# Optimization experiments

Hardware: AMD Instinct MI355X
Metric: run time of the kernel (lower is better)

The kernel has to match this reference:

```python
import jax, jax.numpy as jnp
import numpy as np


def setup_inputs() -> dict:
    key = jax.random.key(0)
    k1, k2, k3, k4, k5 = jax.random.split(key, 5)
    B, N, E, C, O = 4, 10000, 32, 128, 128
    x = jax.random.normal(k1, (B, N, C), dtype=jnp.float32)
    idx = jax.random.randint(k2, (B, N, E), 0, N)
    drop = jax.random.uniform(k3, (B, N, E)) < 0.1
    edge_index = jnp.where(drop, -1, idx).astype(jnp.int64)
    W = jax.random.normal(k4, (2 * C, O), dtype=jnp.float32) * (1.0 / np.sqrt(2 * C))
    b = jax.random.normal(k5, (O,), dtype=jnp.float32) * 0.01
    return {"x": x, "edge_index": edge_index, "W": W, "b": b}


def reference(x, edge_index, W, b):
    B, N, C = x.shape
    E = edge_index.shape[-1]
    # pad a zero node row; -1 indices point at it (torch negative-index semantics)
    padded = jnp.concatenate([x, jnp.zeros((B, 1, C), dtype=x.dtype)], axis=1)  # [B, N+1, C]
    idx = jnp.where(edge_index < 0, N, edge_index)
    neigh = jax.vmap(lambda p, i: p[i])(padded, idx)  # [B, N, E, C]
    x_e = jnp.broadcast_to(x[:, :, None, :], (B, N, E, C))
    feat = jnp.concatenate([x_e, neigh - x_e], axis=-1)  # [B, N, E, 2C]
    h = jax.nn.elu(jnp.einsum('bnec,co->bneo', feat, W) + b)  # [B, N, E, O]
    h = jnp.where((edge_index != -1)[..., None], h, -jnp.inf)
    return jnp.max(h, axis=2)  # [B, N, O]
```

## Files before the change

kernel.cpp:

```cpp
#include <hip/hip_runtime.h>
#include <math.h>

#define BATCH 4
#define NNODE 10000
#define EDIM  32
#define CDIM  128
#define ODIM  128
#define MTOT  (BATCH * NNODE)

typedef __attribute__((ext_vector_type(8))) short bf16x8;
typedef __attribute__((ext_vector_type(4))) float f32x4;

__device__ __forceinline__ unsigned short f2bf(float f) {
    unsigned u = __float_as_uint(f);
    u += 0x7fffu + ((u >> 16) & 1u);
    return (unsigned short)(u >> 16);
}

__global__ __launch_bounds__(256) void prep_w(
    const float* __restrict__ W, unsigned short* __restrict__ Bcat)
{
    int gid = blockIdx.x * 256 + threadIdx.x;
    int n = gid >> 7;
    int k = gid & 127;
    float v;
    if (n < 128) v = W[(size_t)k * ODIM + n] - W[(size_t)(k + 128) * ODIM + n];
    else         v = W[(size_t)(k + 128) * ODIM + (n - 128)];
    Bcat[(size_t)n * CDIM + k] = f2bf(v);
}

__global__ __launch_bounds__(256) void gemm_mfma(
    const float* __restrict__ x,
    const unsigned short* __restrict__ Bcat,
    const float* __restrict__ bias,
    float* __restrict__ U,
    unsigned short* __restrict__ T)
{
    const int m0   = blockIdx.x * 64;
    const int wv   = threadIdx.x >> 6;
    const int lane = threadIdx.x & 63;
    const int l16  = lane & 15;
    const int quad = lane >> 4;
    const int nq   = wv * 64;

    f32x4 acc[4][4];
    #pragma unroll
    for (int i = 0; i < 4; i++)
        #pragma unroll
        for (int j = 0; j < 4; j++) acc[i][j] = (f32x4){0.f, 0.f, 0.f, 0.f};

    const float* xb = x + (size_t)m0 * CDIM;

    #pragma unroll
    for (int ks = 0; ks < 4; ks++) {
        const int kb = ks * 32 + quad * 8;

        bf16x8 bfr[4];
        #pragma unroll
        for (int ct = 0; ct < 4; ct++)
            bfr[ct] = *(const bf16x8*)(Bcat + (size_t)(nq + ct * 16 + l16) * CDIM + kb);

        bf16x8 afr[4];
        #pragma unroll
        for (int rt = 0; rt < 4; rt++) {
            const float* ap = xb + (size_t)(rt * 16 + l16) * CDIM + kb;
            float4 a0 = *(const float4*)ap;
            float4 a1 = *(const float4*)(ap + 4);
            bf16x8 v;
            v[0] = (short)f2bf(a0.x); v[1] = (short)f2bf(a0.y);
            v[2] = (short)f2bf(a0.z); v[3] = (short)f2bf(a0.w);
            v[4] = (short)f2bf(a1.x); v[5] = (short)f2bf(a1.y);
            v[6] = (short)f2bf(a1.z); v[7] = (short)f2bf(a1.w);
            afr[rt] = v;
        }

        #pragma unroll
        for (int rt = 0; rt < 4; rt++)
            #pragma unroll
            for (int ct = 0; ct < 4; ct++)
                acc[rt][ct] = __builtin_amdgcn_mfma_f32_16x16x32_bf16(
                    afr[rt], bfr[ct], acc[rt][ct], 0, 0, 0);
    }

    if (wv < 2) {
        #pragma unroll
        for (int ct = 0; ct < 4; ct++) {
            int n = nq + ct * 16 + l16;
            float bb = bias[n];
            #pragma unroll
            for (int rt = 0; rt < 4; rt++) {
                int row = m0 + rt * 16 + quad * 4;
                #pragma unroll
                for (int r = 0; r < 4; r++)
                    U[(size_t)(row + r) * ODIM + n] = acc[rt][ct][r] + bb;
            }
        }
    } else {
        #pragma unroll
        for (int ct = 0; ct < 4; ct++) {
            int n = nq - 128 + ct * 16 + l16;
            #pragma unroll
            for (int rt = 0; rt < 4; rt++) {
                int row = m0 + rt * 16 + quad * 4;
                #pragma unroll
                for (int r = 0; r < 4; r++)
                    T[(size_t)(row + r) * ODIM + n] = f2bf(acc[rt][ct][r]);
            }
        }
    }
}

__global__ __launch_bounds__(256) void gather_max(
    const int* __restrict__ idx,
    const float* Uin,
    const unsigned short* __restrict__ T,
    float* out)
{
    const int g    = blockIdx.x;
    const int b    = (g & 7) >> 1;
    const int wb   = (g >> 3) * 2 + (g & 1);
    const int wave = threadIdx.x >> 6;
    const int lane = threadIdx.x & 63;
    const int node = b * NNODE + wb * 4 + wave;

    __shared__ int sidx[4][EDIM];
    if (threadIdx.x < 4 * EDIM) {
        int w = threadIdx.x >> 5;
        int e = threadIdx.x & 31;
        sidx[w][e] = idx[(size_t)(b * NNODE + wb * 4 + w) * EDIM + e];
    }
    __syncthreads();

    const unsigned short* tb = T + (size_t)b * NNODE * ODIM;
    const int o2 = lane * 2;

    int      jv[EDIM];
    unsigned vv[EDIM];
    #pragma unroll
    for (int e = 0; e < EDIM; e++) {
        int j = sidx[wave][e];
        jv[e] = j;
        int jc = j < 0 ? 0 : j;
        vv[e] = *(const unsigned*)(tb + (size_t)jc * ODIM + o2);
    }

    float m0 = -INFINITY, m1 = -INFINITY;
    bool any = false;
    #pragma unroll
    for (int e = 0; e < EDIM; e++) {
        if (jv[e] >= 0) {
            any = true;
            m0 = fmaxf(m0, __uint_as_float(vv[e] << 16));
            m1 = fmaxf(m1, __uint_as_float(vv[e] & 0xffff0000u));
        }
    }

    float2 uv = *(const float2*)&Uin[(size_t)node * ODIM + o2];
    float r0, r1;
    if (any) {
        float s0 = uv.x + m0;
        float s1 = uv.y + m1;
        r0 = s0 > 0.f ? s0 : __expf(s0) - 1.f;
        r1 = s1 > 0.f ? s1 : __expf(s1) - 1.f;
    } else {
        r0 = -INFINITY;
        r1 = -INFINITY;
    }
    *(float2*)&out[(size_t)node * ODIM + o2] = make_float2(r0, r1);
}

extern "C" void kernel_launch(void* const* d_in, const int* in_sizes, int n_in,
                              void* d_out, int out_size, void* d_ws, size_t ws_size,
                              hipStream_t stream) {
    const float* x    = (const float*)d_in[0];
    const int*   idx  = (const int*)d_in[1];
    const float* W    = (const float*)d_in[2];
    const float* bias = (const float*)d_in[3];
    float* out        = (float*)d_out;

    const size_t tBytes = (size_t)MTOT * ODIM * sizeof(unsigned short);
    const size_t uBytes = (size_t)MTOT * ODIM * sizeof(float);
    unsigned short* T = (unsigned short*)d_ws;
    float* U;
    unsigned short* Bcat;
    if (ws_size >= tBytes + uBytes + 256 * CDIM * sizeof(unsigned short)) {
        U    = (float*)((char*)d_ws + tBytes);
        Bcat = (unsigned short*)((char*)d_ws + tBytes + uBytes);
    } else {
        U    = out;
        Bcat = (unsigned short*)((char*)d_ws + tBytes);
    }

    prep_w   <<<128,       256, 0, stream>>>(W, Bcat);
    gemm_mfma<<<MTOT / 64, 256, 0, stream>>>(x, Bcat, bias, U, T);
    gather_max<<<MTOT / 4, 256, 0, stream>>>(idx, U, T, out);
}
```

Measured before the change: 128.9 us.

## Stage x in swizzled LDS for GEMM, widen gather loads with sentinel row

The GEMM kernel now converts each 64-row x tile to bf16 once and stores it in an XOR-swizzled shared-memory tile. Each wave then reads its A fragments from there instead of reloading and reconverting x from global memory in every wave. The gather kernel handles 16 nodes per block, with 16 lanes per node each loading 16 bytes (8 bf16 channels). Padded edges are redirected to an appended sentinel row filled with -inf, which removes the per-edge branch. This adds LDS use and a dependency on the sentinel row being written by prep_w.

```diff
diff --git a/kernel.cpp b/kernel.cpp
--- a/kernel.cpp
+++ b/kernel.cpp
@@ -18,7 +18,8 @@
 }
 
 __global__ __launch_bounds__(256) void prep_w(
-    const float* __restrict__ W, unsigned short* __restrict__ Bcat)
+    const float* __restrict__ W, unsigned short* __restrict__ Bcat,
+    unsigned short* __restrict__ Tsent)
 {
     int gid = blockIdx.x * 256 + threadIdx.x;
     int n = gid >> 7;
@@ -27,6 +28,7 @@
     if (n < 128) v = W[(size_t)k * ODIM + n] - W[(size_t)(k + 128) * ODIM + n];
     else         v = W[(size_t)(k + 128) * ODIM + (n - 128)];
     Bcat[(size_t)n * CDIM + k] = f2bf(v);
+    if (gid < ODIM) Tsent[gid] = 0xFF80;
 }
 
 __global__ __launch_bounds__(256) void gemm_mfma(
@@ -36,20 +38,34 @@
     float* __restrict__ U,
     unsigned short* __restrict__ T)
 {
+    __shared__ unsigned short As[64 * 128];
+
+    const int tid  = threadIdx.x;
     const int m0   = blockIdx.x * 64;
-    const int wv   = threadIdx.x >> 6;
-    const int lane = threadIdx.x & 63;
+    const int wv   = tid >> 6;
+    const int lane = tid & 63;
     const int l16  = lane & 15;
     const int quad = lane >> 4;
     const int nq   = wv * 64;
 
+    #pragma unroll
+    for (int i = 0; i < 8; i++) {
+        int lin = i * 256 + tid;
+        int row = lin >> 5;
+        int f4  = lin & 31;
+        float4 v = *(const float4*)&x[(size_t)(m0 + row) * CDIM + f4 * 4];
+        ushort4 h;
+        h.x = f2bf(v.x); h.y = f2bf(v.y); h.z = f2bf(v.z); h.w = f2bf(v.w);
+        int kblk = f4 >> 1, half = f4 & 1;
+        *(ushort4*)((char*)As + row * 256 + (((kblk ^ (row & 15)) << 4) + half * 8)) = h;
+    }
+    __syncthreads();
+
     f32x4 acc[4][4];
     #pragma unroll
     for (int i = 0; i < 4; i++)
         #pragma unroll
         for (int j = 0; j < 4; j++) acc[i][j] = (f32x4){0.f, 0.f, 0.f, 0.f};
-
-    const float* xb = x + (size_t)m0 * CDIM;
 
     #pragma unroll
     for (int ks = 0; ks < 4; ks++) {
@@ -63,15 +79,9 @@
         bf16x8 afr[4];
         #pragma unroll
         for (int rt = 0; rt < 4; rt++) {
-            const float* ap = xb + (size_t)(rt * 16 + l16) * CDIM + kb;
-            float4 a0 = *(const float4*)ap;
-            float4 a1 = *(const float4*)(ap + 4);
-            bf16x8 v;
-            v[0] = (short)f2bf(a0.x); v[1] = (short)f2bf(a0.y);
-            v[2] = (short)f2bf(a0.z); v[3] = (short)f2bf(a0.w);
-            v[4] = (short)f2bf(a1.x); v[5] = (short)f2bf(a1.y);
-            v[6] = (short)f2bf(a1.z); v[7] = (short)f2bf(a1.w);
-            afr[rt] = v;
+            int row  = rt * 16 + l16;
+            int kblk = ks * 4 + quad;
+            afr[rt] = *(const bf16x8*)((char*)As + row * 256 + ((kblk ^ l16) << 4));
         }
 
         #pragma unroll
@@ -116,57 +126,71 @@
     const unsigned short* __restrict__ T,
     float* out)
 {
-    const int g    = blockIdx.x;
-    const int b    = (g & 7) >> 1;
-    const int wb   = (g >> 3) * 2 + (g & 1);
-    const int wave = threadIdx.x >> 6;
-    const int lane = threadIdx.x & 63;
-    const int node = b * NNODE + wb * 4 + wave;
-
-    __shared__ int sidx[4][EDIM];
-    if (threadIdx.x < 4 * EDIM) {
-        int w = threadIdx.x >> 5;
-        int e = threadIdx.x & 31;
-        sidx[w][e] = idx[(size_t)(b * NNODE + wb * 4 + w) * EDIM + e];
+    __shared__ int sidx[16][EDIM];
+
+    const int g   = blockIdx.x;
+    const int b   = g & 3;
+    const int nb0 = (g >> 2) * 16;
+    const int tid = threadIdx.x;
+    const int sent = NNODE * (BATCH - b);
+
+    #pragma unroll
+    for (int i = 0; i < 2; i++) {
+        int lin = i * 256 + tid;
+        int n = lin >> 5, e = lin & 31;
+        int j = idx[(size_t)(b * NNODE + nb0 + n) * EDIM + e];
+        sidx[n][e] = (j < 0) ? sent : j;
     }
     __syncthreads();
 
+    const int wv   = tid >> 6;
+    const int lane = tid & 63;
+    const int q4   = lane >> 4;
+    const int l16  = lane & 15;
+    const int myn  = wv * 4 + q4;
+    const int node = b * NNODE + nb0 + myn;
     const unsigned short* tb = T + (size_t)b * NNODE * ODIM;
-    const int o2 = lane * 2;
-
-    int      jv[EDIM];
-    unsigned vv[EDIM];
-    #pragma unroll
-    for (int e = 0; e < EDIM; e++) {
-        int j = sidx[wave][e];
-        jv[e] = j;
-        int jc = j < 0 ? 0 : j;
-        vv[e] = *(const unsigned*)(tb + (size_t)jc * ODIM + o2);
-    }
-
-    float m0 = -INFINITY, m1 = -INFINITY;
-    bool any = false;
-    #pragma unroll
-    for (int e = 0; e < EDIM; e++) {
-        if (jv[e] >= 0) {
-            any = true;
-            m0 = fmaxf(m0, __uint_as_float(vv[e] << 16));
-            m1 = fmaxf(m1, __uint_as_float(vv[e] & 0xffff0000u));
-        }
-    }
-
-    float2 uv = *(const float2*)&Uin[(size_t)node * ODIM + o2];
-    float r0, r1;
-    if (any) {
-        float s0 = uv.x + m0;
-        float s1 = uv.y + m1;
-        r0 = s0 > 0.f ? s0 : __expf(s0) - 1.f;
-        r1 = s1 > 0.f ? s1 : __expf(s1) - 1.f;
-    } else {
-        r0 = -INFINITY;
-        r1 = -INFINITY;
-    }
-    *(float2*)&out[(size_t)node * ODIM + o2] = make_float2(r0, r1);
+    const int o8 = l16 * 8;
+
+    float m[8];
+    #pragma unroll
+    for (int i = 0; i < 8; i++) m[i] = -INFINITY;
+
+    #pragma unroll
+    for (int e0 = 0; e0 < EDIM; e0 += 8) {
+        uint4 v[8];
+        #pragma unroll
+        for (int q = 0; q < 8; q++) {
+            int j = sidx[myn][e0 + q];
+            v[q] = *(const uint4*)(tb + (size_t)j * ODIM + o8);
+        }
+        #pragma unroll
+        for (int q = 0; q < 8; q++) {
+            m[0] = fmaxf(m[0], __uint_as_float(v[q].x << 16));
+            m[1] = fmaxf(m[1], __uint_as_float(v[q].x & 0xffff0000u));
+            m[2] = fmaxf(m[2], __uint_as_float(v[q].y << 16));
+            m[3] = fmaxf(m[3], __uint_as_float(v[q].y & 0xffff0000u));
+            m[4] = fmaxf(m[4], __uint_as_float(v[q].z << 16));
+            m[5] = fmaxf(m[5], __uint_as_float(v[q].z & 0xffff0000u));
+            m[6] = fmaxf(m[6], __uint_as_float(v[q].w << 16));
+            m[7] = fmaxf(m[7], __uint_as_float(v[q].w & 0xffff0000u));
+        }
+    }
+
+    const bool any = m[0] > -INFINITY;
+    float4 u0 = *(const float4*)&Uin[(size_t)node * ODIM + o8];
+    float4 u1 = *(const float4*)&Uin[(size_t)node * ODIM + o8 + 4];
+    float uu[8] = {u0.x, u0.y, u0.z, u0.w, u1.x, u1.y, u1.z, u1.w};
+    float r[8];
+    #pragma unroll
+    for (int i = 0; i < 8; i++) {
+        float s = uu[i] + m[i];
+        r[i] = any ? (s > 0.f ? s : __expf(s) - 1.f) : -INFINITY;
+    }
+    float4 w0 = make_float4(r[0], r[1], r[2], r[3]);
+    float4 w1 = make_float4(r[4], r[5], r[6], r[7]);
+    *(float4*)&out[(size_t)node * ODIM + o8]     = w0;
+    *(float4*)&out[(size_t)node * ODIM + o8 + 4] = w1;
 }
 
 extern "C" void kernel_launch(void* const* d_in, const int* in_sizes, int n_in,
@@ -178,20 +202,22 @@
     const float* bias = (const float*)d_in[3];
     float* out        = (float*)d_out;
 
-    const size_t tBytes = (size_t)MTOT * ODIM * sizeof(unsigned short);
+    const size_t tBytes = (size_t)(MTOT + 1) * ODIM * sizeof(unsigned short);
     const size_t uBytes = (size_t)MTOT * ODIM * sizeof(float);
+    const size_t bBytes = (size_t)256 * CDIM * sizeof(unsigned short);
     unsigned short* T = (unsigned short*)d_ws;
     float* U;
     unsigned short* Bcat;
-    if (ws_size >= tBytes + uBytes + 256 * CDIM * sizeof(unsigned short)) {
+    if (ws_size >= tBytes + uBytes + bBytes) {
         U    = (float*)((char*)d_ws + tBytes);
         Bcat = (unsigned short*)((char*)d_ws + tBytes + uBytes);
     } else {
         U    = out;
         Bcat = (unsigned short*)((char*)d_ws + tBytes);
     }
-
-    prep_w   <<<128,       256, 0, stream>>>(W, Bcat);
-    gemm_mfma<<<MTOT / 64, 256, 0, stream>>>(x, Bcat, bias, U, T);
-    gather_max<<<MTOT / 4, 256, 0, stream>>>(idx, U, T, out);
-}
+    unsigned short* Tsent = T + (size_t)MTOT * ODIM;
+
+    prep_w    <<<128,        256, 0, stream>>>(W, Bcat, Tsent);
+    gemm_mfma <<<MTOT / 64,  256, 0, stream>>>(x, Bcat, bias, U, T);
+    gather_max<<<MTOT / 16,  256, 0, stream>>>(idx, U, T, out);
+}
```

Measured after the change: 110.4 us. 14.3% less time.
